# Performance work log

Measured on AMD Instinct MI355X. Metric: run time of the kernel, lower is better.

The kernel has to match this reference:

```python
import jax, jax.numpy as jnp
import numpy as np

N_NODES = 50000
N_EDGES = 800000
N_GRAPHS = 50
IN_FEATS = 128
H1_FEATS = 64
OUT_FEATS = 32
GAT_SLOPE = 0.2   # DGL GATConv default negative_slope
LRELU_SLOPE = 0.01  # F.leaky_relu default


def setup_inputs() -> dict:
    key = jax.random.key(0)
    ks = jax.random.split(key, 12)
    x = jax.random.normal(ks[0], (N_NODES, IN_FEATS), jnp.float32)
    src = jax.random.randint(ks[1], (N_EDGES,), 0, N_NODES)
    dst = jax.random.randint(ks[2], (N_EDGES,), 0, N_NODES)
    graph_id = jnp.sort(jax.random.randint(ks[3], (N_NODES,), 0, N_GRAPHS))
    s1 = 1.0 / np.sqrt(IN_FEATS)
    s2 = 1.0 / np.sqrt(H1_FEATS)
    W1 = jax.random.normal(ks[4], (IN_FEATS, H1_FEATS), jnp.float32) * s1
    al1 = jax.random.normal(ks[5], (H1_FEATS,), jnp.float32) * s2
    ar1 = jax.random.normal(ks[6], (H1_FEATS,), jnp.float32) * s2
    b1 = jnp.zeros((H1_FEATS,), jnp.float32)
    W2 = jax.random.normal(ks[7], (H1_FEATS, OUT_FEATS), jnp.float32) * s2
    al2 = jax.random.normal(ks[8], (OUT_FEATS,), jnp.float32) * (1.0 / np.sqrt(OUT_FEATS))
    ar2 = jax.random.normal(ks[9], (OUT_FEATS,), jnp.float32) * (1.0 / np.sqrt(OUT_FEATS))
    b2 = jnp.zeros((OUT_FEATS,), jnp.float32)
    return {"x": x, "src": src, "dst": dst, "graph_id": graph_id,
            "W1": W1, "al1": al1, "ar1": ar1, "b1": b1,
            "W2": W2, "al2": al2, "ar2": ar2, "b2": b2}


def _gat_layer(h, src, dst, W, al, ar, b, n_nodes):
    # single-head DGL GATConv (feat_drop=attn_drop=0, bias added post-aggregation)
    z = h @ W                                   # (N, out)
    el = z @ al                                 # (N,) left attention logits
    er = z @ ar                                 # (N,) right attention logits
    e = jax.nn.leaky_relu(el[src] + er[dst], GAT_SLOPE)     # (E,)
    m = jax.ops.segment_max(e, dst, num_segments=n_nodes)  # per-dst max for stable softmax
    p = jnp.exp(e - m[dst])
    s = jax.ops.segment_sum(p, dst, num_segments=n_nodes)
    alpha = p / s[dst]                          # edge softmax over incoming edges
    out = jax.ops.segment_sum(alpha[:, None] * z[src], dst, num_segments=n_nodes)
    return out + b


def reference(x, src, dst, graph_id, W1, al1, ar1, b1, W2, al2, ar2, b2):
    n = x.shape[0]
    h = jax.nn.leaky_relu(_gat_layer(x, src, dst, W1, al1, ar1, b1, n), LRELU_SLOPE)
    h = jax.nn.leaky_relu(_gat_layer(h, src, dst, W2, al2, ar2, b2, n), LRELU_SLOPE)
    # dgl.mean_nodes: per-graph mean over nodes
    cnt = jax.ops.segment_sum(jnp.ones((n,), h.dtype), graph_id, num_segments=N_GRAPHS)
    pooled = jax.ops.segment_sum(h, graph_id, num_segments=N_GRAPHS) / jnp.maximum(cnt, 1.0)[:, None]
    return pooled
```

## Files before the change

### kernel.cpp

```cpp
#include <hip/hip_runtime.h>
#include <math.h>

#define NN 50000
#define NE 800000
#define NG 50
#define F0 128
#define F1 64
#define F2 32
#define NPB 256
#define NBK 196
#define CHUNK 4096
#define NC 196

__device__ __forceinline__ float lrelu(float v, float slope) {
    return v > 0.0f ? v : v * slope;
}

__global__ __launch_bounds__(256) void gemm1_kernel(
    const float* __restrict__ x, const float* __restrict__ W,
    const float* __restrict__ al, const float* __restrict__ ar,
    float* __restrict__ z, float* __restrict__ el, float* __restrict__ er)
{
    __shared__ float Ws[F0 * F1];
    __shared__ float xs[32][F0];
    int tid = threadIdx.x;
    int r0 = blockIdx.x * 32;

    {
        const float4* W4 = reinterpret_cast<const float4*>(W);
        float4* Ws4 = reinterpret_cast<float4*>(Ws);
        #pragma unroll
        for (int i = 0; i < 8; ++i) Ws4[tid + i * 256] = W4[tid + i * 256];
    }
    {
        float4 zero = {0.f, 0.f, 0.f, 0.f};
        #pragma unroll
        for (int i = 0; i < 4; ++i) {
            int s = tid + i * 256;
            int row = s >> 5, c4 = s & 31;
            int grow = r0 + row;
            float4 v = (grow < NN)
                ? reinterpret_cast<const float4*>(x)[(size_t)grow * 32 + c4] : zero;
            *reinterpret_cast<float4*>(&xs[row][c4 * 4]) = v;
        }
    }
    __syncthreads();

    int j = tid & 63, rg = tid >> 6;
    float acc[8] = {0.f, 0.f, 0.f, 0.f, 0.f, 0.f, 0.f, 0.f};
    for (int k4 = 0; k4 < F0 / 4; ++k4) {
        float w0 = Ws[(k4 * 4 + 0) * F1 + j];
        float w1 = Ws[(k4 * 4 + 1) * F1 + j];
        float w2 = Ws[(k4 * 4 + 2) * F1 + j];
        float w3 = Ws[(k4 * 4 + 3) * F1 + j];
        #pragma unroll
        for (int r = 0; r < 8; ++r) {
            float4 xv = *reinterpret_cast<const float4*>(&xs[rg * 8 + r][k4 * 4]);
            acc[r] = fmaf(xv.x, w0, fmaf(xv.y, w1, fmaf(xv.z, w2, fmaf(xv.w, w3, acc[r]))));
        }
    }

    float a_l = al[j], a_r = ar[j];
    #pragma unroll
    for (int r = 0; r < 8; ++r) {
        int row = r0 + rg * 8 + r;
        if (row < NN) z[(size_t)row * F1 + j] = acc[r];
        float pl = acc[r] * a_l, pr = acc[r] * a_r;
        #pragma unroll
        for (int mm = 1; mm < 64; mm <<= 1) {
            pl += __shfl_xor(pl, mm);
            pr += __shfl_xor(pr, mm);
        }
        if (j == 0 && row < NN) { el[row] = pl; er[row] = pr; }
    }
}

__global__ __launch_bounds__(256) void gemm2_kernel(
    const float* __restrict__ h, const float* __restrict__ W,
    const float* __restrict__ al, const float* __restrict__ ar,
    float* __restrict__ z, float* __restrict__ el, float* __restrict__ er)
{
    __shared__ float Ws[F1 * F2];
    __shared__ float xs[64][F1];
    int tid = threadIdx.x;
    int r0 = blockIdx.x * 64;

    {
        const float4* W4 = reinterpret_cast<const float4*>(W);
        float4* Ws4 = reinterpret_cast<float4*>(Ws);
        #pragma unroll
        for (int i = 0; i < 2; ++i) Ws4[tid + i * 256] = W4[tid + i * 256];
    }
    {
        float4 zero = {0.f, 0.f, 0.f, 0.f};
        #pragma unroll
        for (int i = 0; i < 4; ++i) {
            int s = tid + i * 256;
            int row = s >> 4, c4 = s & 15;
            int grow = r0 + row;
            float4 v = (grow < NN)
                ? reinterpret_cast<const float4*>(h)[(size_t)grow * 16 + c4] : zero;
            *reinterpret_cast<float4*>(&xs[row][c4 * 4]) = v;
        }
    }
    __syncthreads();

    int j = tid & 31, rg = tid >> 5;
    float acc[8] = {0.f, 0.f, 0.f, 0.f, 0.f, 0.f, 0.f, 0.f};
    for (int k4 = 0; k4 < F1 / 4; ++k4) {
        float w0 = Ws[(k4 * 4 + 0) * F2 + j];
        float w1 = Ws[(k4 * 4 + 1) * F2 + j];
        float w2 = Ws[(k4 * 4 + 2) * F2 + j];
        float w3 = Ws[(k4 * 4 + 3) * F2 + j];
        #pragma unroll
        for (int r = 0; r < 8; ++r) {
            float4 xv = *reinterpret_cast<const float4*>(&xs[rg * 8 + r][k4 * 4]);
            acc[r] = fmaf(xv.x, w0, fmaf(xv.y, w1, fmaf(xv.z, w2, fmaf(xv.w, w3, acc[r]))));
        }
    }

    float a_l = al[j], a_r = ar[j];
    #pragma unroll
    for (int r = 0; r < 8; ++r) {
        int row = r0 + rg * 8 + r;
        if (row < NN) z[(size_t)row * F2 + j] = acc[r];
        float pl = acc[r] * a_l, pr = acc[r] * a_r;
        #pragma unroll
        for (int mm = 1; mm < 32; mm <<= 1) {
            pl += __shfl_xor(pl, mm);
            pr += __shfl_xor(pr, mm);
        }
        if (j == 0 && row < NN) { el[row] = pl; er[row] = pr; }
    }
}


__global__ __launch_bounds__(256) void p1_hist_kernel(
    const int* __restrict__ dst, int* __restrict__ hist)
{
    __shared__ int h[NBK];
    int c = blockIdx.x;
    if (threadIdx.x < NBK) h[threadIdx.x] = 0;
    __syncthreads();
    int e0 = c * CHUNK;
    int e1 = (e0 + CHUNK < NE) ? e0 + CHUNK : NE;
    for (int e = e0 + threadIdx.x; e < e1; e += 256)
        atomicAdd(&h[dst[e] >> 8], 1);
    __syncthreads();
    if (threadIdx.x < NBK) hist[threadIdx.x * NC + c] = h[threadIdx.x];
}

__global__ __launch_bounds__(256) void p2a_scan_kernel(
    int* __restrict__ hist, int* __restrict__ btot)
{
    __shared__ int t[256];
    int b = blockIdx.x;
    int v = (threadIdx.x < NC) ? hist[b * NC + threadIdx.x] : 0;
    t[threadIdx.x] = v;
    __syncthreads();
    for (int off = 1; off < 256; off <<= 1) {
        int u = (threadIdx.x >= off) ? t[threadIdx.x - off] : 0;
        __syncthreads();
        t[threadIdx.x] += u;
        __syncthreads();
    }
    if (threadIdx.x < NC) hist[b * NC + threadIdx.x] = t[threadIdx.x] - v;
    if (threadIdx.x == 255) btot[b] = t[255];
}

__global__ __launch_bounds__(256) void p2b_scan_kernel(
    const int* __restrict__ btot, int* __restrict__ bstart, int* __restrict__ row_start)
{
    __shared__ int t[256];
    int v = (threadIdx.x < NBK) ? btot[threadIdx.x] : 0;
    t[threadIdx.x] = v;
    __syncthreads();
    for (int off = 1; off < 256; off <<= 1) {
        int u = (threadIdx.x >= off) ? t[threadIdx.x - off] : 0;
        __syncthreads();
        t[threadIdx.x] += u;
        __syncthreads();
    }
    if (threadIdx.x < NBK) bstart[threadIdx.x] = t[threadIdx.x] - v;
    if (threadIdx.x == NBK) bstart[NBK] = NE;
    if (threadIdx.x == 0) row_start[NN] = NE;
}

__global__ __launch_bounds__(256) void p3_part_kernel(
    const int* __restrict__ src, const int* __restrict__ dst,
    const int* __restrict__ hist, const int* __restrict__ bstart,
    int2* __restrict__ part)
{
    __shared__ int base[NBK];
    __shared__ int cnt[NBK];
    int c = blockIdx.x;
    if (threadIdx.x < NBK) {
        base[threadIdx.x] = hist[threadIdx.x * NC + c] + bstart[threadIdx.x];
        cnt[threadIdx.x] = 0;
    }
    __syncthreads();
    int e0 = c * CHUNK;
    int e1 = (e0 + CHUNK < NE) ? e0 + CHUNK : NE;
    for (int e = e0 + threadIdx.x; e < e1; e += 256) {
        int s = src[e], d = dst[e];
        int b = d >> 8;
        int r = atomicAdd(&cnt[b], 1);
        part[base[b] + r] = make_int2(s, d);
    }
}

__global__ __launch_bounds__(256) void p4_fill_kernel(
    const int2* __restrict__ part, const int* __restrict__ bstart,
    int* __restrict__ row_start, int* __restrict__ srcs)
{
    __shared__ int deg[NPB];
    __shared__ int off[NPB];
    __shared__ int cnt[NPB];
    int b = blockIdx.x;
    int lo = bstart[b], hi = bstart[b + 1];
    deg[threadIdx.x] = 0;
    cnt[threadIdx.x] = 0;
    __syncthreads();
    for (int i = lo + threadIdx.x; i < hi; i += 256)
        atomicAdd(&deg[part[i].y & (NPB - 1)], 1);
    __syncthreads();
    int v = deg[threadIdx.x];
    off[threadIdx.x] = v;
    __syncthreads();
    for (int o = 1; o < 256; o <<= 1) {
        int u = (threadIdx.x >= o) ? off[threadIdx.x - o] : 0;
        __syncthreads();
        off[threadIdx.x] += u;
        __syncthreads();
    }
    int ex = off[threadIdx.x] - v;
    __syncthreads();
    off[threadIdx.x] = ex;
    __syncthreads();
    int node = b * NPB + threadIdx.x;
    if (node < NN) row_start[node] = lo + ex;
    for (int i = lo + threadIdx.x; i < hi; i += 256) {
        int2 e = part[i];
        int n = e.y & (NPB - 1);
        int r = atomicAdd(&cnt[n], 1);
        srcs[lo + off[n] + r] = e.x;
    }
}

__global__ __launch_bounds__(256) void gat_agg64_kernel(
    const int* __restrict__ row_start, const int* __restrict__ srcs,
    const float* __restrict__ el, const float* __restrict__ er,
    const float* __restrict__ z, const float* __restrict__ b,
    float* __restrict__ out, float slope_out)
{
    int node = (blockIdx.x * 256 + threadIdx.x) >> 6;
    if (node >= NN) return;
    int lane = threadIdx.x & 63;
    int g = lane >> 4, c = lane & 15;
    int beg = row_start[node], end = row_start[node + 1];
    float erd = er[node];

    int i0 = beg + lane;
    float v0 = -INFINITY;
    if (i0 < end) v0 = lrelu(el[srcs[i0]] + erd, 0.2f);
    float lm = v0;
    for (int i = i0 + 64; i < end; i += 64)
        lm = fmaxf(lm, lrelu(el[srcs[i]] + erd, 0.2f));
    #pragma unroll
    for (int mm = 1; mm < 64; mm <<= 1) lm = fmaxf(lm, __shfl_xor(lm, mm));

    float preg = 0.f, ls = 0.f;
    if (i0 < end) { preg = __expf(v0 - lm); ls = preg; }
    for (int i = i0 + 64; i < end; i += 64)
        ls += __expf(lrelu(el[srcs[i]] + erd, 0.2f) - lm);
    #pragma unroll
    for (int mm = 1; mm < 64; mm <<= 1) ls += __shfl_xor(ls, mm);
    float inv_s = (ls > 0.f) ? 1.0f / ls : 0.f;

    const float4* z4 = reinterpret_cast<const float4*>(z);
    float4 acc = {0.f, 0.f, 0.f, 0.f};
    for (int ib = beg; ib < end; ib += 4) {
        int i = ib + g;
        int j = i - beg;
        float pv = __shfl(preg, j & 63);
        if (i < end) {
            int sn = srcs[i];
            if (j >= 64) pv = __expf(lrelu(el[sn] + erd, 0.2f) - lm);
            float alpha = pv * inv_s;
            float4 zv = z4[(size_t)sn * 16 + c];
            acc.x = fmaf(alpha, zv.x, acc.x);
            acc.y = fmaf(alpha, zv.y, acc.y);
            acc.z = fmaf(alpha, zv.z, acc.z);
            acc.w = fmaf(alpha, zv.w, acc.w);
        }
    }
    #pragma unroll
    for (int mm = 16; mm < 64; mm <<= 1) {
        acc.x += __shfl_xor(acc.x, mm);
        acc.y += __shfl_xor(acc.y, mm);
        acc.z += __shfl_xor(acc.z, mm);
        acc.w += __shfl_xor(acc.w, mm);
    }
    if (g == 0) {
        float4 bb = reinterpret_cast<const float4*>(b)[c];
        float4 o;
        o.x = lrelu(acc.x + bb.x, slope_out);
        o.y = lrelu(acc.y + bb.y, slope_out);
        o.z = lrelu(acc.z + bb.z, slope_out);
        o.w = lrelu(acc.w + bb.w, slope_out);
        reinterpret_cast<float4*>(out)[(size_t)node * 16 + c] = o;
    }
}

__global__ __launch_bounds__(256) void gat_agg32_kernel(
    const int* __restrict__ row_start, const int* __restrict__ srcs,
    const float* __restrict__ el, const float* __restrict__ er,
    const float* __restrict__ z, const float* __restrict__ b,
    float* __restrict__ out, float slope_out)
{
    int node = (blockIdx.x * 256 + threadIdx.x) >> 5;
    if (node >= NN) return;
    int sub = threadIdx.x & 31;
    int base = threadIdx.x & 32;
    int g = sub >> 3, c = sub & 7;
    int beg = row_start[node], end = row_start[node + 1];
    float erd = er[node];

    int i0 = beg + sub;
    float v0 = -INFINITY;
    if (i0 < end) v0 = lrelu(el[srcs[i0]] + erd, 0.2f);
    float lm = v0;
    for (int i = i0 + 32; i < end; i += 32)
        lm = fmaxf(lm, lrelu(el[srcs[i]] + erd, 0.2f));
    #pragma unroll
    for (int mm = 1; mm < 32; mm <<= 1) lm = fmaxf(lm, __shfl_xor(lm, mm));

    float preg = 0.f, ls = 0.f;
    if (i0 < end) { preg = __expf(v0 - lm); ls = preg; }
    for (int i = i0 + 32; i < end; i += 32)
        ls += __expf(lrelu(el[srcs[i]] + erd, 0.2f) - lm);
    #pragma unroll
    for (int mm = 1; mm < 32; mm <<= 1) ls += __shfl_xor(ls, mm);
    float inv_s = (ls > 0.f) ? 1.0f / ls : 0.f;

    const float4* z4 = reinterpret_cast<const float4*>(z);
    float4 acc = {0.f, 0.f, 0.f, 0.f};
    for (int ib = beg; ib < end; ib += 4) {
        int i = ib + g;
        int j = i - beg;
        float pv = __shfl(preg, base | (j & 31));
        if (i < end) {
            int sn = srcs[i];
            if (j >= 32) pv = __expf(lrelu(el[sn] + erd, 0.2f) - lm);
            float alpha = pv * inv_s;
            float4 zv = z4[(size_t)sn * 8 + c];
            acc.x = fmaf(alpha, zv.x, acc.x);
            acc.y = fmaf(alpha, zv.y, acc.y);
            acc.z = fmaf(alpha, zv.z, acc.z);
            acc.w = fmaf(alpha, zv.w, acc.w);
        }
    }
    #pragma unroll
    for (int mm = 8; mm < 32; mm <<= 1) {
        acc.x += __shfl_xor(acc.x, mm);
        acc.y += __shfl_xor(acc.y, mm);
        acc.z += __shfl_xor(acc.z, mm);
        acc.w += __shfl_xor(acc.w, mm);
    }
    if (g == 0) {
        float4 bb = reinterpret_cast<const float4*>(b)[c];
        float4 o;
        o.x = lrelu(acc.x + bb.x, slope_out);
        o.y = lrelu(acc.y + bb.y, slope_out);
        o.z = lrelu(acc.z + bb.z, slope_out);
        o.w = lrelu(acc.w + bb.w, slope_out);
        reinterpret_cast<float4*>(out)[(size_t)node * 8 + c] = o;
    }
}

__global__ __launch_bounds__(256) void pool_kernel(
    const float* __restrict__ h2, const int* __restrict__ gid, float* __restrict__ out)
{
    int g = blockIdx.x;
    int lo = 0, hi = NN;
    while (lo < hi) { int mid = (lo + hi) >> 1; if (gid[mid] < g) lo = mid + 1; else hi = mid; }
    int start = lo;
    hi = NN;
    while (lo < hi) { int mid = (lo + hi) >> 1; if (gid[mid] < g + 1) lo = mid + 1; else hi = mid; }
    int end = lo;

    int f = threadIdx.x & 31, r = threadIdx.x >> 5;
    float acc = 0.f;
    for (int n = start + r; n < end; n += 8) acc += h2[(size_t)n * F2 + f];
    __shared__ float red[256];
    red[threadIdx.x] = acc;
    __syncthreads();
    for (int st = 128; st >= 32; st >>= 1) {
        if (threadIdx.x < st) red[threadIdx.x] += red[threadIdx.x + st];
        __syncthreads();
    }
    if (threadIdx.x < 32) {
        float cnt = (float)(end - start);
        out[g * F2 + threadIdx.x] = red[threadIdx.x] / fmaxf(cnt, 1.0f);
    }
}

extern "C" void kernel_launch(void* const* d_in, const int* in_sizes, int n_in,
                              void* d_out, int out_size, void* d_ws, size_t ws_size,
                              hipStream_t stream)
{
    const float* x   = (const float*)d_in[0];
    const int*   src = (const int*)d_in[1];
    const int*   dst = (const int*)d_in[2];
    const int*   gid = (const int*)d_in[3];
    const float* W1  = (const float*)d_in[4];
    const float* al1 = (const float*)d_in[5];
    const float* ar1 = (const float*)d_in[6];
    const float* b1  = (const float*)d_in[7];
    const float* W2  = (const float*)d_in[8];
    const float* al2 = (const float*)d_in[9];
    const float* ar2 = (const float*)d_in[10];
    const float* b2  = (const float*)d_in[11];
    float* out = (float*)d_out;

    float* ws   = (float*)d_ws;
    float* z1   = ws;
    float* h1   = z1 + (size_t)NN * F1;
    float* z2   = h1 + (size_t)NN * F1;
    float* h2   = z2 + (size_t)NN * F2;
    float* el   = h2 + (size_t)NN * F2;
    float* er   = el + NN;
    int* row_start = (int*)(er + NN);
    int* srcs      = row_start + NN + 1;
    int* hist      = srcs + NE;
    int* btot      = hist + NBK * NC;
    int* bstart    = btot + NBK;
    int2* part = reinterpret_cast<int2*>(z1);

    p1_hist_kernel<<<NC, 256, 0, stream>>>(dst, hist);
    p2a_scan_kernel<<<NBK, 256, 0, stream>>>(hist, btot);
    p2b_scan_kernel<<<1, 256, 0, stream>>>(btot, bstart, row_start);
    p3_part_kernel<<<NC, 256, 0, stream>>>(src, dst, hist, bstart, part);
    p4_fill_kernel<<<NBK, 256, 0, stream>>>(part, bstart, row_start, srcs);

    gemm1_kernel<<<(NN + 31) / 32, 256, 0, stream>>>(x, W1, al1, ar1, z1, el, er);
    gat_agg64_kernel<<<(NN * 64 + 255) / 256, 256, 0, stream>>>(
        row_start, srcs, el, er, z1, b1, h1, 0.01f);

    gemm2_kernel<<<(NN + 63) / 64, 256, 0, stream>>>(h1, W2, al2, ar2, z2, el, er);
    gat_agg32_kernel<<<(NN * 32 + 255) / 256, 256, 0, stream>>>(
        row_start, srcs, el, er, z2, b2, h2, 0.01f);

    pool_kernel<<<NG, 256, 0, stream>>>(h2, gid, out);
}
```

Before: 286.8 us.

## Fuse all GAT pipeline stages into one cooperative persistent kernel with grid syncs

Replaces the ten separate kernel launches with a single cooperative kernel of 512 persistent blocks. Stages are separated by grid.sync, and the CSR histogram runs concurrently with the first GEMM on disjoint block ranges. The aggregation loops are unrolled to process two edges per iteration for more memory-level parallelism. The partition buffer moves out of z1 so the GEMM can overlap with CSR construction. This trades launch overhead and gaps between kernels for grid-barrier cost and fewer resident blocks, and the old kernels remain as a fallback if the cooperative launch fails.

```diff
diff --git a/kernel.cpp b/kernel.cpp
--- a/kernel.cpp
+++ b/kernel.cpp
@@ -1,5 +1,8 @@
 #include <hip/hip_runtime.h>
+#include <hip/hip_cooperative_groups.h>
 #include <math.h>
+
+namespace cg = cooperative_groups;
 
 #define NN 50000
 #define NE 800000
@@ -11,10 +14,418 @@
 #define NBK 196
 #define CHUNK 4096
 #define NC 196
+#define NCSR 196
+#define NTILE1 1563
+#define NTILE2 782
+#define NBLK 512
 
 __device__ __forceinline__ float lrelu(float v, float slope) {
     return v > 0.0f ? v : v * slope;
 }
+
+struct MegaParams {
+    const float* x; const int* src; const int* dst; const int* gid;
+    const float* W1; const float* al1; const float* ar1; const float* b1;
+    const float* W2; const float* al2; const float* ar2; const float* b2;
+    float* out;
+    float* z1; float* h1; float* z2; float* h2; float* el; float* er;
+    int* row_start; int* srcs; int* hist; int* btot; int* bstart;
+    int2* part;
+};
+
+__global__ __launch_bounds__(256, 2) void mega_kernel(MegaParams P)
+{
+    cg::grid_group grid = cg::this_grid();
+    const int tid = threadIdx.x;
+    const int bid = blockIdx.x;
+    const int nblk = gridDim.x;
+    __shared__ __align__(16) char smraw[49152];
+
+    if (bid < NCSR) {
+        int* h = (int*)smraw;
+        for (int c = bid; c < NC; c += NCSR) {
+            if (tid < NBK) h[tid] = 0;
+            __syncthreads();
+            int e0 = c * CHUNK;
+            int e1 = (e0 + CHUNK < NE) ? e0 + CHUNK : NE;
+            for (int e = e0 + tid; e < e1; e += 256)
+                atomicAdd(&h[P.dst[e] >> 8], 1);
+            __syncthreads();
+            if (tid < NBK) P.hist[tid * NC + c] = h[tid];
+            __syncthreads();
+        }
+    } else {
+        float* Ws = (float*)smraw;
+        float (*xs)[F0] = (float (*)[F0])(smraw + F0 * F1 * 4);
+        const float4* W4 = (const float4*)P.W1;
+        float4* Ws4 = (float4*)Ws;
+        #pragma unroll
+        for (int i = 0; i < 8; ++i) Ws4[tid + i * 256] = W4[tid + i * 256];
+        __syncthreads();
+        int j = tid & 63, rg = tid >> 6;
+        float a_l = P.al1[j], a_r = P.ar1[j];
+        for (int tile = bid - NCSR; tile < NTILE1; tile += nblk - NCSR) {
+            int r0 = tile * 32;
+            float4 zero = {0.f, 0.f, 0.f, 0.f};
+            #pragma unroll
+            for (int i2 = 0; i2 < 4; ++i2) {
+                int s = tid + i2 * 256;
+                int row = s >> 5, c4 = s & 31;
+                int grow = r0 + row;
+                float4 v = (grow < NN)
+                    ? ((const float4*)P.x)[(size_t)grow * 32 + c4] : zero;
+                *(float4*)&xs[row][c4 * 4] = v;
+            }
+            __syncthreads();
+            float acc[8] = {0.f, 0.f, 0.f, 0.f, 0.f, 0.f, 0.f, 0.f};
+            for (int k4 = 0; k4 < F0 / 4; ++k4) {
+                float w0 = Ws[(k4 * 4 + 0) * F1 + j];
+                float w1 = Ws[(k4 * 4 + 1) * F1 + j];
+                float w2 = Ws[(k4 * 4 + 2) * F1 + j];
+                float w3 = Ws[(k4 * 4 + 3) * F1 + j];
+                #pragma unroll
+                for (int r = 0; r < 8; ++r) {
+                    float4 xv = *(const float4*)&xs[rg * 8 + r][k4 * 4];
+                    acc[r] = fmaf(xv.x, w0, fmaf(xv.y, w1, fmaf(xv.z, w2, fmaf(xv.w, w3, acc[r]))));
+                }
+            }
+            #pragma unroll
+            for (int r = 0; r < 8; ++r) {
+                int row = r0 + rg * 8 + r;
+                if (row < NN) P.z1[(size_t)row * F1 + j] = acc[r];
+                float pl = acc[r] * a_l, pr = acc[r] * a_r;
+                #pragma unroll
+                for (int mm = 1; mm < 64; mm <<= 1) {
+                    pl += __shfl_xor(pl, mm);
+                    pr += __shfl_xor(pr, mm);
+                }
+                if (j == 0 && row < NN) { P.el[row] = pl; P.er[row] = pr; }
+            }
+            __syncthreads();
+        }
+    }
+    grid.sync();
+
+    if (bid < NBK) {
+        int* t = (int*)smraw;
+        int v = (tid < NC) ? P.hist[bid * NC + tid] : 0;
+        t[tid] = v;
+        __syncthreads();
+        for (int off = 1; off < 256; off <<= 1) {
+            int u = (tid >= off) ? t[tid - off] : 0;
+            __syncthreads();
+            t[tid] += u;
+            __syncthreads();
+        }
+        if (tid < NC) P.hist[bid * NC + tid] = t[tid] - v;
+        if (tid == 255) P.btot[bid] = t[255];
+    }
+    grid.sync();
+
+    if (bid == 0) {
+        int* t = (int*)smraw;
+        int v = (tid < NBK) ? P.btot[tid] : 0;
+        t[tid] = v;
+        __syncthreads();
+        for (int off = 1; off < 256; off <<= 1) {
+            int u = (tid >= off) ? t[tid - off] : 0;
+            __syncthreads();
+            t[tid] += u;
+            __syncthreads();
+        }
+        if (tid < NBK) P.bstart[tid] = t[tid] - v;
+        if (tid == NBK) P.bstart[NBK] = NE;
+        if (tid == 0) P.row_start[NN] = NE;
+    }
+    grid.sync();
+
+    if (bid < NCSR) {
+        int* base = (int*)smraw;
+        int* cnt  = base + NBK;
+        for (int cc = bid; cc < NC; cc += NCSR) {
+            if (tid < NBK) {
+                base[tid] = P.hist[tid * NC + cc] + P.bstart[tid];
+                cnt[tid] = 0;
+            }
+            __syncthreads();
+            int e0 = cc * CHUNK;
+            int e1 = (e0 + CHUNK < NE) ? e0 + CHUNK : NE;
+            for (int e = e0 + tid; e < e1; e += 256) {
+                int s = P.src[e], d = P.dst[e];
+                int b = d >> 8;
+                int r = atomicAdd(&cnt[b], 1);
+                P.part[base[b] + r] = make_int2(s, d);
+            }
+            __syncthreads();
+        }
+    }
+    grid.sync();
+
+    if (bid < NBK) {
+        int* deg = (int*)smraw;
+        int* off = deg + NPB;
+        int* cnt = off + NPB;
+        int lo = P.bstart[bid], hi = P.bstart[bid + 1];
+        deg[tid] = 0;
+        cnt[tid] = 0;
+        __syncthreads();
+        for (int i = lo + tid; i < hi; i += 256)
+            atomicAdd(&deg[P.part[i].y & (NPB - 1)], 1);
+        __syncthreads();
+        int v = deg[tid];
+        off[tid] = v;
+        __syncthreads();
+        for (int o = 1; o < 256; o <<= 1) {
+            int u = (tid >= o) ? off[tid - o] : 0;
+            __syncthreads();
+            off[tid] += u;
+            __syncthreads();
+        }
+        int ex = off[tid] - v;
+        __syncthreads();
+        off[tid] = ex;
+        __syncthreads();
+        int node = bid * NPB + tid;
+        if (node < NN) P.row_start[node] = lo + ex;
+        for (int i = lo + tid; i < hi; i += 256) {
+            int2 e = P.part[i];
+            int n = e.y & (NPB - 1);
+            int r = atomicAdd(&cnt[n], 1);
+            P.srcs[lo + off[n] + r] = e.x;
+        }
+    }
+    grid.sync();
+
+    {
+        const float4* z4 = (const float4*)P.z1;
+        int lane = tid & 63;
+        int w = tid >> 6;
+        int g = lane >> 4, c = lane & 15;
+        for (int node = bid * 4 + w; node < NN; node += nblk * 4) {
+            int beg = P.row_start[node], end = P.row_start[node + 1];
+            float erd = P.er[node];
+            int i0 = beg + lane;
+            float v0 = -INFINITY;
+            if (i0 < end) v0 = lrelu(P.el[P.srcs[i0]] + erd, 0.2f);
+            float lm = v0;
+            for (int i = i0 + 64; i < end; i += 64)
+                lm = fmaxf(lm, lrelu(P.el[P.srcs[i]] + erd, 0.2f));
+            #pragma unroll
+            for (int mm = 1; mm < 64; mm <<= 1) lm = fmaxf(lm, __shfl_xor(lm, mm));
+            float preg = 0.f, ls = 0.f;
+            if (i0 < end) { preg = __expf(v0 - lm); ls = preg; }
+            for (int i = i0 + 64; i < end; i += 64)
+                ls += __expf(lrelu(P.el[P.srcs[i]] + erd, 0.2f) - lm);
+            #pragma unroll
+            for (int mm = 1; mm < 64; mm <<= 1) ls += __shfl_xor(ls, mm);
+            float inv_s = (ls > 0.f) ? 1.0f / ls : 0.f;
+
+            float4 acc = {0.f, 0.f, 0.f, 0.f};
+            int ib = beg;
+            for (; ib + 8 <= end; ib += 8) {
+                int ia = ib + g, ic = ib + 4 + g;
+                int ja = ia - beg, jc = ic - beg;
+                float pva = __shfl(preg, ja & 63);
+                float pvc = __shfl(preg, jc & 63);
+                int sna = P.srcs[ia], snc = P.srcs[ic];
+                if (ja >= 64) pva = __expf(lrelu(P.el[sna] + erd, 0.2f) - lm);
+                if (jc >= 64) pvc = __expf(lrelu(P.el[snc] + erd, 0.2f) - lm);
+                float4 zva = z4[(size_t)sna * 16 + c];
+                float4 zvc = z4[(size_t)snc * 16 + c];
+                float aa = pva * inv_s, ac = pvc * inv_s;
+                acc.x = fmaf(aa, zva.x, fmaf(ac, zvc.x, acc.x));
+                acc.y = fmaf(aa, zva.y, fmaf(ac, zvc.y, acc.y));
+                acc.z = fmaf(aa, zva.z, fmaf(ac, zvc.z, acc.z));
+                acc.w = fmaf(aa, zva.w, fmaf(ac, zvc.w, acc.w));
+            }
+            for (; ib < end; ib += 4) {
+                int i = ib + g, jj = i - beg;
+                float pv = __shfl(preg, jj & 63);
+                if (i < end) {
+                    int sn = P.srcs[i];
+                    if (jj >= 64) pv = __expf(lrelu(P.el[sn] + erd, 0.2f) - lm);
+                    float alpha = pv * inv_s;
+                    float4 zv = z4[(size_t)sn * 16 + c];
+                    acc.x = fmaf(alpha, zv.x, acc.x);
+                    acc.y = fmaf(alpha, zv.y, acc.y);
+                    acc.z = fmaf(alpha, zv.z, acc.z);
+                    acc.w = fmaf(alpha, zv.w, acc.w);
+                }
+            }
+            #pragma unroll
+            for (int mm = 16; mm < 64; mm <<= 1) {
+                acc.x += __shfl_xor(acc.x, mm);
+                acc.y += __shfl_xor(acc.y, mm);
+                acc.z += __shfl_xor(acc.z, mm);
+                acc.w += __shfl_xor(acc.w, mm);
+            }
+            if (g == 0) {
+                float4 bb = ((const float4*)P.b1)[c];
+                float4 o;
+                o.x = lrelu(acc.x + bb.x, 0.01f);
+                o.y = lrelu(acc.y + bb.y, 0.01f);
+                o.z = lrelu(acc.z + bb.z, 0.01f);
+                o.w = lrelu(acc.w + bb.w, 0.01f);
+                ((float4*)P.h1)[(size_t)node * 16 + c] = o;
+            }
+        }
+    }
+    grid.sync();
+
+    {
+        float* Ws = (float*)smraw;
+        float (*xs)[F1] = (float (*)[F1])(smraw + F1 * F2 * 4);
+        const float4* W4 = (const float4*)P.W2;
+        float4* Ws4 = (float4*)Ws;
+        #pragma unroll
+        for (int i = 0; i < 2; ++i) Ws4[tid + i * 256] = W4[tid + i * 256];
+        __syncthreads();
+        int j = tid & 31, rg = tid >> 5;
+        float a_l = P.al2[j], a_r = P.ar2[j];
+        for (int tile = bid; tile < NTILE2; tile += nblk) {
+            int r0 = tile * 64;
+            float4 zero = {0.f, 0.f, 0.f, 0.f};
+            #pragma unroll
+            for (int i2 = 0; i2 < 4; ++i2) {
+                int s = tid + i2 * 256;
+                int row = s >> 4, c4 = s & 15;
+                int grow = r0 + row;
+                float4 v = (grow < NN)
+                    ? ((const float4*)P.h1)[(size_t)grow * 16 + c4] : zero;
+                *(float4*)&xs[row][c4 * 4] = v;
+            }
+            __syncthreads();
+            float acc[8] = {0.f, 0.f, 0.f, 0.f, 0.f, 0.f, 0.f, 0.f};
+            for (int k4 = 0; k4 < F1 / 4; ++k4) {
+                float w0 = Ws[(k4 * 4 + 0) * F2 + j];
+                float w1 = Ws[(k4 * 4 + 1) * F2 + j];
+                float w2 = Ws[(k4 * 4 + 2) * F2 + j];
+                float w3 = Ws[(k4 * 4 + 3) * F2 + j];
+                #pragma unroll
+                for (int r = 0; r < 8; ++r) {
+                    float4 xv = *(const float4*)&xs[rg * 8 + r][k4 * 4];
+                    acc[r] = fmaf(xv.x, w0, fmaf(xv.y, w1, fmaf(xv.z, w2, fmaf(xv.w, w3, acc[r]))));
+                }
+            }
+            #pragma unroll
+            for (int r = 0; r < 8; ++r) {
+                int row = r0 + rg * 8 + r;
+                if (row < NN) P.z2[(size_t)row * F2 + j] = acc[r];
+                float pl = acc[r] * a_l, pr = acc[r] * a_r;
+                #pragma unroll
+                for (int mm = 1; mm < 32; mm <<= 1) {
+                    pl += __shfl_xor(pl, mm);
+                    pr += __shfl_xor(pr, mm);
+                }
+                if (j == 0 && row < NN) { P.el[row] = pl; P.er[row] = pr; }
+            }
+            __syncthreads();
+        }
+    }
+    grid.sync();
+
+    {
+        const float4* z4 = (const float4*)P.z2;
+        int sub = tid & 31;
+        int base = tid & 32;
+        int hw = tid >> 5;
+        int g = sub >> 3, c = sub & 7;
+        for (int node = bid * 8 + hw; node < NN; node += nblk * 8) {
+            int beg = P.row_start[node], end = P.row_start[node + 1];
+            float erd = P.er[node];
+            int i0 = beg + sub;
+            float v0 = -INFINITY;
+            if (i0 < end) v0 = lrelu(P.el[P.srcs[i0]] + erd, 0.2f);
+            float lm = v0;
+            for (int i = i0 + 32; i < end; i += 32)
+                lm = fmaxf(lm, lrelu(P.el[P.srcs[i]] + erd, 0.2f));
+            #pragma unroll
+            for (int mm = 1; mm < 32; mm <<= 1) lm = fmaxf(lm, __shfl_xor(lm, mm));
+            float preg = 0.f, ls = 0.f;
+            if (i0 < end) { preg = __expf(v0 - lm); ls = preg; }
+            for (int i = i0 + 32; i < end; i += 32)
+                ls += __expf(lrelu(P.el[P.srcs[i]] + erd, 0.2f) - lm);
+            #pragma unroll
+            for (int mm = 1; mm < 32; mm <<= 1) ls += __shfl_xor(ls, mm);
+            float inv_s = (ls > 0.f) ? 1.0f / ls : 0.f;
+
+            float4 acc = {0.f, 0.f, 0.f, 0.f};
+            int ib = beg;
+            for (; ib + 8 <= end; ib += 8) {
+                int ia = ib + g, ic = ib + 4 + g;
+                int ja = ia - beg, jc = ic - beg;
+                float pva = __shfl(preg, base | (ja & 31));
+                float pvc = __shfl(preg, base | (jc & 31));
+                int sna = P.srcs[ia], snc = P.srcs[ic];
+                if (ja >= 32) pva = __expf(lrelu(P.el[sna] + erd, 0.2f) - lm);
+                if (jc >= 32) pvc = __expf(lrelu(P.el[snc] + erd, 0.2f) - lm);
+                float4 zva = z4[(size_t)sna * 8 + c];
+                float4 zvc = z4[(size_t)snc * 8 + c];
+                float aa = pva * inv_s, ac = pvc * inv_s;
+                acc.x = fmaf(aa, zva.x, fmaf(ac, zvc.x, acc.x));
+                acc.y = fmaf(aa, zva.y, fmaf(ac, zvc.y, acc.y));
+                acc.z = fmaf(aa, zva.z, fmaf(ac, zvc.z, acc.z));
+                acc.w = fmaf(aa, zva.w, fmaf(ac, zvc.w, acc.w));
+            }
+            for (; ib < end; ib += 4) {
+                int i = ib + g, jj = i - beg;
+                float pv = __shfl(preg, base | (jj & 31));
+                if (i < end) {
+                    int sn = P.srcs[i];
+                    if (jj >= 32) pv = __expf(lrelu(P.el[sn] + erd, 0.2f) - lm);
+                    float alpha = pv * inv_s;
+                    float4 zv = z4[(size_t)sn * 8 + c];
+                    acc.x = fmaf(alpha, zv.x, acc.x);
+                    acc.y = fmaf(alpha, zv.y, acc.y);
+                    acc.z = fmaf(alpha, zv.z, acc.z);
+                    acc.w = fmaf(alpha, zv.w, acc.w);
+                }
+            }
+            #pragma unroll
+            for (int mm = 8; mm < 32; mm <<= 1) {
+                acc.x += __shfl_xor(acc.x, mm);
+                acc.y += __shfl_xor(acc.y, mm);
+                acc.z += __shfl_xor(acc.z, mm);
+                acc.w += __shfl_xor(acc.w, mm);
+            }
+            if (g == 0) {
+                float4 bb = ((const float4*)P.b2)[c];
+                float4 o;
+                o.x = lrelu(acc.x + bb.x, 0.01f);
+                o.y = lrelu(acc.y + bb.y, 0.01f);
+                o.z = lrelu(acc.z + bb.z, 0.01f);
+                o.w = lrelu(acc.w + bb.w, 0.01f);
+                ((float4*)P.h2)[(size_t)node * 8 + c] = o;
+            }
+        }
+    }
+    grid.sync();
+
+    if (bid < NG) {
+        float* red = (float*)smraw;
+        int g = bid;
+        int lo = 0, hi = NN;
+        while (lo < hi) { int mid = (lo + hi) >> 1; if (P.gid[mid] < g) lo = mid + 1; else hi = mid; }
+        int start = lo;
+        hi = NN;
+        while (lo < hi) { int mid = (lo + hi) >> 1; if (P.gid[mid] < g + 1) lo = mid + 1; else hi = mid; }
+        int end = lo;
+        int f = tid & 31, r = tid >> 5;
+        float acc = 0.f;
+        for (int n = start + r; n < end; n += 8) acc += P.h2[(size_t)n * F2 + f];
+        red[tid] = acc;
+        __syncthreads();
+        for (int st = 128; st >= 32; st >>= 1) {
+            if (tid < st) red[tid] += red[tid + st];
+            __syncthreads();
+        }
+        if (tid < 32) {
+            float cnt = (float)(end - start);
+            P.out[g * F2 + tid] = red[tid] / fmaxf(cnt, 1.0f);
+        }
+    }
+}
+
 
 __global__ __launch_bounds__(256) void gemm1_kernel(
     const float* __restrict__ x, const float* __restrict__ W,
@@ -25,7 +436,6 @@
     __shared__ float xs[32][F0];
     int tid = threadIdx.x;
     int r0 = blockIdx.x * 32;
-
     {
         const float4* W4 = reinterpret_cast<const float4*>(W);
         float4* Ws4 = reinterpret_cast<float4*>(Ws);
@@ -45,7 +455,6 @@
         }
     }
     __syncthreads();
-
     int j = tid & 63, rg = tid >> 6;
     float acc[8] = {0.f, 0.f, 0.f, 0.f, 0.f, 0.f, 0.f, 0.f};
     for (int k4 = 0; k4 < F0 / 4; ++k4) {
@@ -59,7 +468,6 @@
             acc[r] = fmaf(xv.x, w0, fmaf(xv.y, w1, fmaf(xv.z, w2, fmaf(xv.w, w3, acc[r]))));
         }
     }
-
     float a_l = al[j], a_r = ar[j];
     #pragma unroll
     for (int r = 0; r < 8; ++r) {
@@ -84,7 +492,6 @@
     __shared__ float xs[64][F1];
     int tid = threadIdx.x;
     int r0 = blockIdx.x * 64;
-
     {
         const float4* W4 = reinterpret_cast<const float4*>(W);
         float4* Ws4 = reinterpret_cast<float4*>(Ws);
@@ -104,7 +511,6 @@
         }
     }
     __syncthreads();
-
     int j = tid & 31, rg = tid >> 5;
     float acc[8] = {0.f, 0.f, 0.f, 0.f, 0.f, 0.f, 0.f, 0.f};
     for (int k4 = 0; k4 < F1 / 4; ++k4) {
@@ -118,7 +524,6 @@
             acc[r] = fmaf(xv.x, w0, fmaf(xv.y, w1, fmaf(xv.z, w2, fmaf(xv.w, w3, acc[r]))));
         }
     }
-
     float a_l = al[j], a_r = ar[j];
     #pragma unroll
     for (int r = 0; r < 8; ++r) {
@@ -133,7 +538,6 @@
         if (j == 0 && row < NN) { el[row] = pl; er[row] = pr; }
     }
 }
-
 
 __global__ __launch_bounds__(256) void p1_hist_kernel(
     const int* __restrict__ dst, int* __restrict__ hist)
@@ -259,7 +663,6 @@
     int g = lane >> 4, c = lane & 15;
     int beg = row_start[node], end = row_start[node + 1];
     float erd = er[node];
-
     int i0 = beg + lane;
     float v0 = -INFINITY;
     if (i0 < end) v0 = lrelu(el[srcs[i0]] + erd, 0.2f);
@@ -268,7 +671,6 @@
         lm = fmaxf(lm, lrelu(el[srcs[i]] + erd, 0.2f));
     #pragma unroll
     for (int mm = 1; mm < 64; mm <<= 1) lm = fmaxf(lm, __shfl_xor(lm, mm));
-
     float preg = 0.f, ls = 0.f;
     if (i0 < end) { preg = __expf(v0 - lm); ls = preg; }
     for (int i = i0 + 64; i < end; i += 64)
@@ -276,7 +678,6 @@
     #pragma unroll
     for (int mm = 1; mm < 64; mm <<= 1) ls += __shfl_xor(ls, mm);
     float inv_s = (ls > 0.f) ? 1.0f / ls : 0.f;
-
     const float4* z4 = reinterpret_cast<const float4*>(z);
     float4 acc = {0.f, 0.f, 0.f, 0.f};
     for (int ib = beg; ib < end; ib += 4) {
@@ -325,7 +726,6 @@
     int g = sub >> 3, c = sub & 7;
     int beg = row_start[node], end = row_start[node + 1];
     float erd = er[node];
-
     int i0 = beg + sub;
     float v0 = -INFINITY;
     if (i0 < end) v0 = lrelu(el[srcs[i0]] + erd, 0.2f);
@@ -334,7 +734,6 @@
         lm = fmaxf(lm, lrelu(el[srcs[i]] + erd, 0.2f));
     #pragma unroll
     for (int mm = 1; mm < 32; mm <<= 1) lm = fmaxf(lm, __shfl_xor(lm, mm));
-
     float preg = 0.f, ls = 0.f;
     if (i0 < end) { preg = __expf(v0 - lm); ls = preg; }
     for (int i = i0 + 32; i < end; i += 32)
@@ -342,7 +741,6 @@
     #pragma unroll
     for (int mm = 1; mm < 32; mm <<= 1) ls += __shfl_xor(ls, mm);
     float inv_s = (ls > 0.f) ? 1.0f / ls : 0.f;
-
     const float4* z4 = reinterpret_cast<const float4*>(z);
     float4 acc = {0.f, 0.f, 0.f, 0.f};
     for (int ib = beg; ib < end; ib += 4) {
@@ -388,7 +786,6 @@
     hi = NN;
     while (lo < hi) { int mid = (lo + hi) >> 1; if (gid[mid] < g + 1) lo = mid + 1; else hi = mid; }
     int end = lo;
-
     int f = threadIdx.x & 31, r = threadIdx.x >> 5;
     float acc = 0.f;
     for (int n = start + r; n < end; n += 8) acc += h2[(size_t)n * F2 + f];
@@ -409,21 +806,7 @@
                               void* d_out, int out_size, void* d_ws, size_t ws_size,
                               hipStream_t stream)
 {
-    const float* x   = (const float*)d_in[0];
-    const int*   src = (const int*)d_in[1];
-    const int*   dst = (const int*)d_in[2];
-    const int*   gid = (const int*)d_in[3];
-    const float* W1  = (const float*)d_in[4];
-    const float* al1 = (const float*)d_in[5];
-    const float* ar1 = (const float*)d_in[6];
-    const float* b1  = (const float*)d_in[7];
-    const float* W2  = (const float*)d_in[8];
-    const float* al2 = (const float*)d_in[9];
-    const float* ar2 = (const float*)d_in[10];
-    const float* b2  = (const float*)d_in[11];
-    float* out = (float*)d_out;
-
-    float* ws   = (float*)d_ws;
+    float* ws = (float*)d_ws;
     float* z1   = ws;
     float* h1   = z1 + (size_t)NN * F1;
     float* z2   = h1 + (size_t)NN * F1;
@@ -435,21 +818,41 @@
     int* hist      = srcs + NE;
     int* btot      = hist + NBK * NC;
     int* bstart    = btot + NBK;
-    int2* part = reinterpret_cast<int2*>(z1);
-
-    p1_hist_kernel<<<NC, 256, 0, stream>>>(dst, hist);
-    p2a_scan_kernel<<<NBK, 256, 0, stream>>>(hist, btot);
-    p2b_scan_kernel<<<1, 256, 0, stream>>>(btot, bstart, row_start);
-    p3_part_kernel<<<NC, 256, 0, stream>>>(src, dst, hist, bstart, part);
-    p4_fill_kernel<<<NBK, 256, 0, stream>>>(part, bstart, row_start, srcs);
-
-    gemm1_kernel<<<(NN + 31) / 32, 256, 0, stream>>>(x, W1, al1, ar1, z1, el, er);
-    gat_agg64_kernel<<<(NN * 64 + 255) / 256, 256, 0, stream>>>(
-        row_start, srcs, el, er, z1, b1, h1, 0.01f);
-
-    gemm2_kernel<<<(NN + 63) / 64, 256, 0, stream>>>(h1, W2, al2, ar2, z2, el, er);
-    gat_agg32_kernel<<<(NN * 32 + 255) / 256, 256, 0, stream>>>(
-        row_start, srcs, el, er, z2, b2, h2, 0.01f);
-
-    pool_kernel<<<NG, 256, 0, stream>>>(h2, gid, out);
-}
+    int2* part     = (int2*)(bstart + NBK + 1);
+
+    MegaParams P;
+    P.x   = (const float*)d_in[0];
+    P.src = (const int*)d_in[1];
+    P.dst = (const int*)d_in[2];
+    P.gid = (const int*)d_in[3];
+    P.W1  = (const float*)d_in[4];
+    P.al1 = (const float*)d_in[5];
+    P.ar1 = (const float*)d_in[6];
+    P.b1  = (const float*)d_in[7];
+    P.W2  = (const float*)d_in[8];
+    P.al2 = (const float*)d_in[9];
+    P.ar2 = (const float*)d_in[10];
+    P.b2  = (const float*)d_in[11];
+    P.out = (float*)d_out;
+    P.z1 = z1; P.h1 = h1; P.z2 = z2; P.h2 = h2; P.el = el; P.er = er;
+    P.row_start = row_start; P.srcs = srcs; P.hist = hist;
+    P.btot = btot; P.bstart = bstart; P.part = part;
+
+    void* args[] = { &P };
+    hipError_t err = hipLaunchCooperativeKernel((void*)mega_kernel, dim3(NBLK),
+                                                dim3(256), args, 0, stream);
+    if (err != hipSuccess) {
+        p1_hist_kernel<<<NC, 256, 0, stream>>>(P.dst, hist);
+        p2a_scan_kernel<<<NBK, 256, 0, stream>>>(hist, btot);
+        p2b_scan_kernel<<<1, 256, 0, stream>>>(btot, bstart, row_start);
+        p3_part_kernel<<<NC, 256, 0, stream>>>(P.src, P.dst, hist, bstart, part);
+        p4_fill_kernel<<<NBK, 256, 0, stream>>>(part, bstart, row_start, srcs);
+        gemm1_kernel<<<NTILE1, 256, 0, stream>>>(P.x, P.W1, P.al1, P.ar1, z1, el, er);
+        gat_agg64_kernel<<<(NN * 64 + 255) / 256, 256, 0, stream>>>(
+            row_start, srcs, el, er, z1, P.b1, h1, 0.01f);
+        gemm2_kernel<<<NTILE2, 256, 0, stream>>>(h1, P.W2, P.al2, P.ar2, z2, el, er);
+        gat_agg32_kernel<<<(NN * 32 + 255) / 256, 256, 0, stream>>>(
+            row_start, srcs, el, er, z2, P.b2, h2, 0.01f);
+        pool_kernel<<<NG, 256, 0, stream>>>(h2, P.gid, P.out);
+    }
+}
```

After: 909.4 us. 217% more time.
